# Kernel tuning notes

Hardware: AMD Instinct MI355X
Metric: run time of the kernel (lower is better)

Reference implementation:

```python
import jax, jax.numpy as jnp
import numpy as np

NUM_HEADS = 4
LN_EPS = 1e-5
NEG_INF = -1e9


def _ln(x, g, b):
    mu = jnp.mean(x, axis=-1, keepdims=True)
    var = jnp.mean(jnp.square(x - mu), axis=-1, keepdims=True)
    return (x - mu) * jax.lax.rsqrt(var + LN_EPS) * g + b


def setup_inputs() -> dict:
    key = jax.random.key(0)
    B, L, D, C, E, T, H, NL, MLP = 1024, 200, 64, 32, 32, 8, 256, 3, 256
    P = D + E            # 96
    KIN = H + 2 * T      # 272
    ks = iter(jax.random.split(key, 64))

    def w(shape, fan_in):
        return jax.random.normal(next(ks), shape, dtype=jnp.float32) / np.sqrt(fan_in)

    inp = {}
    inp['x_u'] = jax.random.normal(next(ks), (B, D), dtype=jnp.float32)
    inp['x_ctx'] = jax.random.normal(next(ks), (B, L, D), dtype=jnp.float32)
    inp['t_ctx'] = jax.random.uniform(next(ks), (B, L), dtype=jnp.float32)
    inp['act_u_idx'] = jax.random.randint(next(ks), (B,), 0, C + 1)
    inp['act_ctx_idx'] = jax.random.randint(next(ks), (B, L), 0, C + 1)
    emb = jax.random.normal(next(ks), (C + 1, E), dtype=jnp.float32)
    inp['emb'] = emb.at[0].set(0.0)  # padding_idx=0
    inp['W_in_self'] = w((P, H), P); inp['b_in_self'] = jnp.zeros((H,), jnp.float32)
    inp['W_in_ctx'] = w((P, H), P); inp['b_in_ctx'] = jnp.zeros((H,), jnp.float32)
    inp['freq'] = jax.random.normal(next(ks), (NL, T), dtype=jnp.float32)
    inp['phase'] = jnp.zeros((NL, T), jnp.float32)
    inp['Wq'] = w((NL, H, H), H)
    inp['Wk'] = w((NL, KIN, H), KIN)
    inp['Wv'] = w((NL, KIN, H), KIN)
    inp['Wres'] = w((NL, H, H), H); inp['bres'] = jnp.zeros((NL, H), jnp.float32)
    inp['Wff1'] = w((NL, H, H), H); inp['bff1'] = jnp.zeros((NL, H), jnp.float32)
    inp['Wff2'] = w((NL, H, H), H); inp['bff2'] = jnp.zeros((NL, H), jnp.float32)
    inp['g1'] = jnp.ones((NL, H), jnp.float32); inp['beta1'] = jnp.zeros((NL, H), jnp.float32)
    inp['g2'] = jnp.ones((NL, H), jnp.float32); inp['beta2'] = jnp.zeros((NL, H), jnp.float32)
    inp['W_ro'] = w((H, MLP), H); inp['b_ro'] = jnp.zeros((MLP,), jnp.float32)
    inp['W_cls'] = w((MLP, C), MLP); inp['b_cls'] = jnp.zeros((C,), jnp.float32)
    inp['W_dt'] = w((MLP, 1), MLP); inp['b_dt'] = jnp.zeros((1,), jnp.float32)
    inp['W_rem'] = w((MLP, 1), MLP); inp['b_rem'] = jnp.zeros((1,), jnp.float32)
    return inp


def reference(x_u, x_ctx, t_ctx, act_u_idx, act_ctx_idx, emb,
              W_in_self, b_in_self, W_in_ctx, b_in_ctx,
              freq, phase, Wq, Wk, Wv, Wres, bres,
              Wff1, bff1, Wff2, bff2, g1, beta1, g2, beta2,
              W_ro, b_ro, W_cls, b_cls, W_dt, b_dt, W_rem, b_rem):
    B, L, _ = x_ctx.shape
    H = W_in_self.shape[1]
    nh = NUM_HEADS
    Dh = H // nh
    scale = np.sqrt(Dh).astype(np.float32)

    mask = act_ctx_idx > 0                                   # (B, L)
    e_u = emb[act_u_idx]                                     # (B, E)
    e_ctx = emb[act_ctx_idx]                                 # (B, L, E)
    xu = jnp.concatenate([x_u, e_u], axis=-1)
    xc = jnp.concatenate([x_ctx, e_ctx], axis=-1)
    h = xu @ W_in_self + b_in_self                           # (B, H)
    ctx = xc @ W_in_ctx + b_in_ctx                           # (B, L, H)

    logt = jnp.log1p(jnp.maximum(t_ctx, 0.0))                # (B, L)
    n_layers = Wq.shape[0]
    for i in range(n_layers):
        z = logt[..., None] * freq[i] + phase[i]             # (B, L, T)
        te = jnp.concatenate([jnp.sin(z), jnp.cos(z)], axis=-1)  # (B, L, 2T)
        kv = jnp.concatenate([ctx, te], axis=-1)             # (B, L, H+2T)
        q = (h @ Wq[i]).reshape(B, nh, Dh)                   # (B, h, d)
        k = (kv @ Wk[i]).reshape(B, L, nh, Dh)               # (B, l, h, d)
        v = (kv @ Wv[i]).reshape(B, L, nh, Dh)
        att_logits = jnp.einsum('bhd,blhd->bhl', q, k) / scale
        att_logits = jnp.where(mask[:, None, :], att_logits, NEG_INF)
        att = jax.nn.softmax(att_logits, axis=-1)            # (B, h, l)
        agg = jnp.einsum('bhl,blhd->bhd', att, v).reshape(B, H)
        z1 = _ln(agg + h @ Wres[i] + bres[i], g1[i], beta1[i])
        ff = jax.nn.relu(z1 @ Wff1[i] + bff1[i]) @ Wff2[i] + bff2[i]
        h = _ln(z1 + ff, g2[i], beta2[i])

    z = jax.nn.relu(h @ W_ro + b_ro)
    logits = z @ W_cls + b_cls
    dt_hat = jax.nn.sigmoid(z @ W_dt + b_dt)
    rem_hat = jax.nn.sigmoid(z @ W_rem + b_rem)
    return (logits, dt_hat, rem_hat)
```

## Files before the change

### kernel.cpp

```cpp
#include <hip/hip_runtime.h>
#include <math.h>

namespace {
constexpr int Bc   = 1024;
constexpr int Lc   = 200;
constexpr int Dc   = 64;
constexpr int Ec   = 32;
constexpr int Pc   = 96;
constexpr int Hc   = 256;
constexpr int Tc   = 8;
constexpr int NLc  = 3;
constexpr int KINc = 272;
constexpr int DHc  = 64;
constexpr int Cc   = 32;
constexpr int QS   = 113;
constexpr int Q4   = 452;
constexpr int QP   = 464;
constexpr int CG   = 112;
constexpr int CGW  = 448;
constexpr int TEBS  = Bc * Lc + 8;
constexpr float LN_EPS_V = 1e-5f;
constexpr float NEG_BIG  = -1e9f;

typedef __attribute__((ext_vector_type(8))) short bf16x8;
typedef __attribute__((ext_vector_type(4))) float f32x4;

__device__ __forceinline__ unsigned short f2bf(float f) {
    union { float f; unsigned int u; } v; v.f = f;
    unsigned int u = v.u;
    unsigned int r = (u + 0x7fffu + ((u >> 16) & 1u)) >> 16;
    return (unsigned short)r;
}
}

__global__ __launch_bounds__(256) void k_kpv(const float* __restrict__ W_in_ctx,
                                             const float* __restrict__ b_in_ctx,
                                             const float* __restrict__ Wv,
                                             const float* __restrict__ Wk,
                                             float* __restrict__ wvp2,
                                             float* __restrict__ kp) {
    int blk = blockIdx.x;
    int i = blk / QS;
    int j = blk - i * QS;
    int t = threadIdx.x;
    __shared__ float wrow[Hc];
    if (j < 96)        wrow[t] = W_in_ctx[j * Hc + t];
    else if (j == 112) wrow[t] = b_in_ctx[t];
    __syncthreads();
    const float* WvL = Wv + (size_t)i * KINc * Hc;
    const float* WkL = Wk + (size_t)i * KINc * Hc;
    float av, ak;
    if (j >= 96 && j < 112) {
        av = WvL[(256 + (j - 96)) * Hc + t];
        ak = WkL[(256 + (j - 96)) * Hc + t];
    } else {
        av = 0.f; ak = 0.f;
        for (int c = 0; c < Hc; ++c) {
            float w = wrow[c];
            av += w * WvL[c * Hc + t];
            ak += w * WkL[c * Hc + t];
        }
    }
    wvp2[(size_t)blk * Hc + t] = av;
    kp[(size_t)blk * Hc + t]   = ak;
}

__global__ __launch_bounds__(256) void k_wbig2(const float* __restrict__ Wq,
                                               const float* __restrict__ kp,
                                               float* __restrict__ wbig) {
    __shared__ float wq_l[64][65];
    __shared__ float kp_l[113][64];
    int blk = blockIdx.x;
    int i = blk >> 4;
    int rem = blk & 15;
    int h = rem >> 2, et = rem & 3;
    int t = threadIdx.x;
    for (int idx = t; idx < 64 * 64; idx += 256) {
        int e = idx >> 6, d = idx & 63;
        wq_l[e][d] = Wq[(size_t)i * Hc * Hc + (size_t)(et * 64 + e) * Hc + h * 64 + d];
    }
    for (int idx = t; idx < 113 * 64; idx += 256) {
        int r = idx >> 6, d = idx & 63;
        kp_l[r][d] = kp[((size_t)i * QS + r) * Hc + h * 64 + d];
    }
    __syncthreads();
    int e  = t & 63;
    int rq = t >> 6;
    for (int r = rq; r < QS; r += 4) {
        float acc = 0.f;
        #pragma unroll
        for (int d = 0; d < 64; ++d) acc += wq_l[e][d] * kp_l[r][d];
        wbig[((size_t)i * Hc + et * 64 + e) * Q4 + h * QS + r] = 0.125f * acc;
    }
}

__global__ __launch_bounds__(64) void k_frag(const float* __restrict__ wvp2,
                                             const float* __restrict__ Wres,
                                             const float* __restrict__ Wff1,
                                             const float* __restrict__ Wff2,
                                             const float* __restrict__ wbig,
                                             unsigned short* __restrict__ wcat2F,
                                             unsigned short* __restrict__ wffF,
                                             unsigned short* __restrict__ wbigF) {
    int blk = blockIdx.x;
    int lane = threadIdx.x;
    unsigned short v[8];
    if (blk < NLc * 192) {
        int i = blk / 192;
        int r = blk - i * 192;
        int kk = r >> 4, ct = r & 15;
        int c = ct * 16 + (lane & 15);
        int kb = kk * 32 + (lane >> 4) * 8;
        #pragma unroll
        for (int j = 0; j < 8; ++j) {
            int k = kb + j;
            float val;
            if (k < 112)      val = wvp2[((size_t)i * QS + k) * Hc + c];
            else if (k < 368) val = Wres[(size_t)i * Hc * Hc + (size_t)(k - 112) * Hc + c];
            else              val = 0.f;
            v[j] = f2bf(val);
        }
        *(uint4*)&wcat2F[(size_t)blk * 64 * 8 + lane * 8] = *(const uint4*)v;
    } else if (blk < NLc * 192 + NLc * 256) {
        int b2 = blk - NLc * 192;
        int i = b2 / 256;
        int rem = b2 - i * 256;
        int w12 = rem >> 7;
        int r = rem & 127;
        int kk = r >> 4, ct = r & 15;
        int c = ct * 16 + (lane & 15);
        int kb = kk * 32 + (lane >> 4) * 8;
        const float* src = (w12 ? Wff2 : Wff1) + (size_t)i * Hc * Hc;
        #pragma unroll
        for (int j = 0; j < 8; ++j) v[j] = f2bf(src[(size_t)(kb + j) * Hc + c]);
        *(uint4*)&wffF[(size_t)b2 * 64 * 8 + lane * 8] = *(const uint4*)v;
    } else {
        int b3 = blk - NLc * 192 - NLc * 256;
        int i = b3 / 232;
        int r = b3 - i * 232;
        int kk = r / 29, ct = r - kk * 29;
        int c = ct * 16 + (lane & 15);
        int kb = kk * 32 + (lane >> 4) * 8;
        #pragma unroll
        for (int j = 0; j < 8; ++j) {
            float val = (c < Q4) ? wbig[((size_t)i * Hc + kb + j) * Q4 + c] : 0.f;
            v[j] = f2bf(val);
        }
        *(uint4*)&wbigF[(size_t)b3 * 64 * 8 + lane * 8] = *(const uint4*)v;
    }
}

__global__ __launch_bounds__(256) void k_h0(const float* __restrict__ x_u,
                                            const int* __restrict__ act_u,
                                            const float* __restrict__ emb,
                                            const float* __restrict__ W,
                                            const float* __restrict__ bias,
                                            float* __restrict__ h) {
    constexpr int R = 16;
    int b0 = blockIdx.x * R;
    int t = threadIdx.x;
    __shared__ float xu[R * Pc];
    for (int idx = t; idx < R * Pc; idx += 256) {
        int r = idx / Pc, j = idx - r * Pc;
        int b = b0 + r;
        float v;
        if (j < Dc) v = x_u[b * Dc + j];
        else        v = emb[act_u[b] * Ec + (j - Dc)];
        xu[idx] = v;
    }
    __syncthreads();
    float acc[R];
    float bb = bias[t];
    #pragma unroll
    for (int r = 0; r < R; ++r) acc[r] = bb;
    for (int j = 0; j < Pc; ++j) {
        float w = W[j * Hc + t];
        #pragma unroll
        for (int r = 0; r < R; ++r) acc[r] += xu[r * Pc + j] * w;
    }
    #pragma unroll
    for (int r = 0; r < R; ++r) h[(b0 + r) * Hc + t] = acc[r];
}

__global__ __launch_bounds__(256) void k_prepx(const float* __restrict__ x_ctx,
                                               const int* __restrict__ act_ctx,
                                               const float* __restrict__ emb,
                                               unsigned short* __restrict__ xtb) {
    int idx = blockIdx.x * 256 + threadIdx.x;
    int row = idx / 12, c8 = idx - row * 12;
    unsigned short v[8];
    if (c8 < 8) {
        const float* s = x_ctx + (size_t)row * Dc + c8 * 8;
        float4 a0 = *(const float4*)s;
        float4 a1 = *(const float4*)(s + 4);
        v[0]=f2bf(a0.x); v[1]=f2bf(a0.y); v[2]=f2bf(a0.z); v[3]=f2bf(a0.w);
        v[4]=f2bf(a1.x); v[5]=f2bf(a1.y); v[6]=f2bf(a1.z); v[7]=f2bf(a1.w);
    } else {
        int a = act_ctx[row];
        const float* s = emb + (size_t)a * Ec + (c8 - 8) * 8;
        float4 e0 = *(const float4*)s;
        float4 e1 = *(const float4*)(s + 4);
        v[0]=f2bf(e0.x); v[1]=f2bf(e0.y); v[2]=f2bf(e0.z); v[3]=f2bf(e0.w);
        v[4]=f2bf(e1.x); v[5]=f2bf(e1.y); v[6]=f2bf(e1.z); v[7]=f2bf(e1.w);
    }
    *(uint4*)&xtb[(size_t)row * 96 + c8 * 8] = *(const uint4*)v;
}

__global__ __launch_bounds__(256) void k_prept(const float* __restrict__ t_ctx,
                                               const float* __restrict__ freq,
                                               const float* __restrict__ phase,
                                               unsigned short* __restrict__ teb,
                                               unsigned short* __restrict__ teTb) {
    __shared__ float lt[Lc];
    int b = blockIdx.x;
    int t = threadIdx.x;
    if (t < Lc) lt[t] = log1pf(fmaxf(t_ctx[b * Lc + t], 0.f));
    __syncthreads();
    for (int idx = t; idx < NLc * Lc; idx += 256) {
        int i = idx / Lc, l = idx - i * Lc;
        float L = lt[l];
        unsigned short v[16];
        #pragma unroll
        for (int j = 0; j < 8; ++j) {
            float z = L * freq[i * Tc + j] + phase[i * Tc + j];
            v[j]     = f2bf(__sinf(z));
            v[8 + j] = f2bf(__cosf(z));
        }
        size_t base = ((size_t)i * TEBS + b * Lc + l) * 16;
        *(uint4*)&teb[base]     = *(const uint4*)v;
        *(uint4*)&teb[base + 8] = *(const uint4*)&v[8];
    }
    for (int idx = t; idx < NLc * 16 * 28; idx += 256) {
        int i  = idx / 448;
        int r2 = idx - i * 448;
        int f  = r2 / 28, ch = r2 - f * 28;
        int l0 = ch * 8;
        float fr = freq[i * Tc + (f & 7)], ph = phase[i * Tc + (f & 7)];
        bool iscos = f >= 8;
        unsigned short v[8];
        #pragma unroll
        for (int k = 0; k < 8; ++k) {
            int l = l0 + k;
            float val = 0.f;
            if (l < Lc) {
                float z = lt[l] * fr + ph;
                val = iscos ? __cosf(z) : __sinf(z);
            }
            v[k] = f2bf(val);
        }
        *(uint4*)&teTb[((size_t)i * Bc * 16 + b * 16 + f) * 224 + l0] = *(const uint4*)v;
    }
}

__global__ __launch_bounds__(256) void k_qk2b(const float* __restrict__ h,
                                              const float* __restrict__ wbig_l,
                                              unsigned short* __restrict__ qk2b) {
    constexpr int R = 4;
    int rb = blockIdx.x & 255;
    int cb = blockIdx.x >> 8;
    int b0 = rb * R;
    int t = threadIdx.x;
    int c = cb * 256 + t;
    __shared__ float hl[R * Hc];
    for (int idx = t; idx < R * Hc; idx += 256) hl[idx] = h[b0 * Hc + idx];
    __syncthreads();
    if (c >= QP) return;
    if (c >= Q4) {
        #pragma unroll
        for (int r = 0; r < R; ++r) qk2b[(size_t)(b0 + r) * QP + c] = 0;
        return;
    }
    float acc[R];
    #pragma unroll
    for (int r = 0; r < R; ++r) acc[r] = 0.f;
    for (int e = 0; e < Hc; ++e) {
        float w = wbig_l[(size_t)e * Q4 + c];
        #pragma unroll
        for (int r = 0; r < R; ++r) acc[r] += hl[r * Hc + e] * w;
    }
    #pragma unroll
    for (int r = 0; r < R; ++r) qk2b[(size_t)(b0 + r) * QP + c] = f2bf(acc[r]);
}

__global__ __launch_bounds__(512) void k_att(const int* __restrict__ act_ctx,
                                             const unsigned short* __restrict__ qk2b,
                                             const unsigned short* __restrict__ xtb,
                                             const unsigned short* __restrict__ teb_l,
                                             const unsigned short* __restrict__ teTb_l,
                                             float* __restrict__ cagg) {
    constexpr int XS = 112;
    __shared__ __align__(16) unsigned short xt[208 * XS];
    __shared__ unsigned short qks[QP];
    __shared__ float S[4][208];
    __shared__ unsigned short Pl[16][232];
    int b = blockIdx.x;
    int t = threadIdx.x;
    int wv = t >> 6, lane = t & 63;
    int kg = lane >> 4;

    if (t < QP / 2) ((unsigned int*)qks)[t] = ((const unsigned int*)(qk2b + (size_t)b * QP))[t];
    for (int idx = t; idx < 16 * 29; idx += 512) {
        int row = idx / 29, c8 = idx - row * 29;
        uint4 z = {0, 0, 0, 0};
        *(uint4*)&Pl[row][c8 * 8] = z;
    }
    const unsigned short* xrow = xtb + (size_t)b * Lc * 96;
    for (int idx = t; idx < Lc * 12; idx += 512) {
        int l = idx / 12, c8 = idx - l * 12;
        uint4 v = *(const uint4*)(xrow + (size_t)l * 96 + c8 * 8);
        *(uint4*)&xt[l * XS + c8 * 8] = v;
    }
    for (int idx = t; idx < 8 * 12; idx += 512) {
        int l = 200 + idx / 12, c8 = idx - (idx / 12) * 12;
        uint4 z = {0, 0, 0, 0};
        *(uint4*)&xt[l * XS + c8 * 8] = z;
    }
    __syncthreads();

    bf16x8 bfr[4];
    {
        int h = lane & 15;
        int kb = kg * 8;
        #pragma unroll
        for (int kk = 0; kk < 4; ++kk) {
            unsigned short tmp[8];
            #pragma unroll
            for (int j = 0; j < 8; ++j) {
                int k = kk * 32 + kb + j;
                tmp[j] = (h < 4 && k < QS) ? qks[h * QS + k] : (unsigned short)0;
            }
            bfr[kk] = *(const bf16x8*)tmp;
        }
    }

    const unsigned short* terow = teb_l + (size_t)b * Lc * 16;
    for (int tile = wv; tile < 13; tile += 8) {
        int r = tile * 16 + (lane & 15);
        bf16x8 a0 = *(const bf16x8*)&xt[r * XS + kg * 8];
        bf16x8 a1 = *(const bf16x8*)&xt[r * XS + 32 + kg * 8];
        bf16x8 a2 = *(const bf16x8*)&xt[r * XS + 64 + kg * 8];
        bf16x8 a3;
        if (kg < 2) {
            a3 = *(const bf16x8*)(terow + (size_t)r * 16 + kg * 8);
        } else if (kg == 2) {
            unsigned short tmp[8] = {0x3F80u, 0, 0, 0, 0, 0, 0, 0};
            a3 = *(const bf16x8*)tmp;
        } else {
            bf16x8 z = {0, 0, 0, 0, 0, 0, 0, 0};
            a3 = z;
        }
        f32x4 acc = {0.f, 0.f, 0.f, 0.f};
        acc = __builtin_amdgcn_mfma_f32_16x16x32_bf16(a0, bfr[0], acc, 0, 0, 0);
        acc = __builtin_amdgcn_mfma_f32_16x16x32_bf16(a1, bfr[1], acc, 0, 0, 0);
        acc = __builtin_amdgcn_mfma_f32_16x16x32_bf16(a2, bfr[2], acc, 0, 0, 0);
        acc = __builtin_amdgcn_mfma_f32_16x16x32_bf16(a3, bfr[3], acc, 0, 0, 0);
        int h = lane & 15;
        if (h < 4) {
            int rb = tile * 16 + kg * 4;
            #pragma unroll
            for (int q = 0; q < 4; ++q) S[h][rb + q] = acc[q];
        }
    }
    __syncthreads();

    if (wv < 4) {
        int h = wv;
        float lv[4];
        #pragma unroll
        for (int k = 0; k < 4; ++k) {
            int l = lane + 64 * k;
            if (l < Lc) lv[k] = (act_ctx[b * Lc + l] > 0) ? S[h][l] : NEG_BIG;
            else        lv[k] = -INFINITY;
        }
        float m = fmaxf(fmaxf(lv[0], lv[1]), fmaxf(lv[2], lv[3]));
        #pragma unroll
        for (int off = 32; off >= 1; off >>= 1) m = fmaxf(m, __shfl_xor(m, off));
        float p[4];
        float ssum = 0.f;
        #pragma unroll
        for (int k = 0; k < 4; ++k) {
            int l = lane + 64 * k;
            p[k] = (l < Lc) ? __expf(lv[k] - m) : 0.f;
            ssum += p[k];
        }
        #pragma unroll
        for (int off = 32; off >= 1; off >>= 1) ssum += __shfl_xor(ssum, off);
        float sinv = 1.f / ssum;
        #pragma unroll
        for (int k = 0; k < 4; ++k) {
            int l = lane + 64 * k;
            if (l < Lc) Pl[wv][l] = f2bf(p[k] * sinv);
        }
    }
    __syncthreads();

    const unsigned short* teT = teTb_l + (size_t)b * 16 * 224;
    if (wv < 7) {
        int tile = wv;
        int n = lane & 15;
        f32x4 acc = {0.f, 0.f, 0.f, 0.f};
        #pragma unroll
        for (int kk = 0; kk < 7; ++kk) {
            bf16x8 a = *(const bf16x8*)&Pl[lane & 15][kk * 32 + kg * 8];
            bf16x8 bb;
            if (tile < 6) {
                unsigned short tmp[8];
                #pragma unroll
                for (int jj = 0; jj < 8; ++jj)
                    tmp[jj] = xt[(kk * 32 + kg * 8 + jj) * XS + tile * 16 + n];
                bb = *(const bf16x8*)tmp;
            } else {
                bb = *(const bf16x8*)(teT + (size_t)n * 224 + kk * 32 + kg * 8);
            }
            acc = __builtin_amdgcn_mfma_f32_16x16x32_bf16(a, bb, acc, 0, 0, 0);
        }
        if (kg == 0) {
            #pragma unroll
            for (int q = 0; q < 4; ++q)
                cagg[(size_t)b * CGW + q * CG + tile * 16 + n] = acc[q];
        }
    }
}

__global__ __launch_bounds__(512) void k_postq(const float* __restrict__ cagg,
                                               float* __restrict__ h,
                                               const float* __restrict__ wvp2L,
                                               const unsigned short* __restrict__ wcat2F_l,
                                               const unsigned short* __restrict__ wff1F_l,
                                               const unsigned short* __restrict__ wff2F_l,
                                               const float* __restrict__ bresL,
                                               const float* __restrict__ bff1L,
                                               const float* __restrict__ bff2L,
                                               const float* __restrict__ g1L,
                                               const float* __restrict__ beta1L,
                                               const float* __restrict__ g2L,
                                               const float* __restrict__ beta2L,
                                               const unsigned short* __restrict__ wbigF_next,
                                               unsigned short* __restrict__ qk2b) {
    __shared__ __align__(16) unsigned short Xa[16 * 712];
    __shared__ float z1f[16 * 260];
    __shared__ __align__(16) unsigned short z1n[16 * 264];
    __shared__ __align__(16) unsigned short fb16[16 * 264];
    int r0 = blockIdx.x * 16;
    int t = threadIdx.x;
    int wv = t >> 6, lane = t & 63;
    int n = lane & 15, kg = lane >> 4;
    const bf16x8 zf = {0, 0, 0, 0, 0, 0, 0, 0};

    for (int idx = t; idx < 16 * 704; idx += 512) {
        int r = idx / 704, c = idx - r * 704;
        float v = (c < 448) ? cagg[(size_t)(r0 + r) * CGW + c]
                            : h[(size_t)(r0 + r) * Hc + (c - 448)];
        Xa[r * 712 + c] = f2bf(v);
    }
    __syncthreads();

    {
        int hh = wv >> 1;
        f32x4 acc0 = {0.f,0.f,0.f,0.f}, acc1 = {0.f,0.f,0.f,0.f};
        #pragma unroll
        for (int kk = 0; kk < 12; ++kk) {
            int k0 = kk * 32 + kg * 8;
            bf16x8 a;
            if (k0 < 112)      a = *(const bf16x8*)&Xa[(lane & 15) * 712 + hh * 112 + k0];
            else if (k0 < 368) a = *(const bf16x8*)&Xa[(lane & 15) * 712 + 448 + (k0 - 112)];
            else               a = zf;
            bf16x8 b0 = *(const bf16x8*)(wcat2F_l + (((size_t)kk * 16 + wv * 2) * 64 + lane) * 8);
            bf16x8 b1 = *(const bf16x8*)(wcat2F_l + (((size_t)kk * 16 + wv * 2 + 1) * 64 + lane) * 8);
            acc0 = __builtin_amdgcn_mfma_f32_16x16x32_bf16(a, b0, acc0, 0, 0, 0);
            acc1 = __builtin_amdgcn_mfma_f32_16x16x32_bf16(a, b1, acc1, 0, 0, 0);
        }
        int c0 = (wv * 2) * 16 + n, c1 = (wv * 2 + 1) * 16 + n;
        float bi0 = bresL[c0] + wvp2L[112 * Hc + c0];
        float bi1 = bresL[c1] + wvp2L[112 * Hc + c1];
        #pragma unroll
        for (int q = 0; q < 4; ++q) {
            z1f[(kg * 4 + q) * 260 + c0] = acc0[q] + bi0;
            z1f[(kg * 4 + q) * 260 + c1] = acc1[q] + bi1;
        }
    }
    __syncthreads();
    if (wv < 4) {
        int row = wv * 4 + kg;
        float sm = 0.f, sq = 0.f, vals[16];
        #pragma unroll
        for (int s = 0; s < 16; ++s) {
            float v = z1f[row * 260 + n + 16 * s];
            vals[s] = v; sm += v; sq += v * v;
        }
        #pragma unroll
        for (int off = 8; off >= 1; off >>= 1) { sm += __shfl_xor(sm, off); sq += __shfl_xor(sq, off); }
        float mu = sm * (1.f / 256.f);
        float rstd = rsqrtf(sq * (1.f / 256.f) - mu * mu + LN_EPS_V);
        #pragma unroll
        for (int s = 0; s < 16; ++s) {
            int c = n + 16 * s;
            float v = (vals[s] - mu) * rstd * g1L[c] + beta1L[c];
            z1f[row * 260 + c] = v;
            z1n[row * 264 + c] = f2bf(v);
        }
    }
    __syncthreads();
    {
        f32x4 acc0 = {0.f,0.f,0.f,0.f}, acc1 = {0.f,0.f,0.f,0.f};
        for (int kk = 0; kk < 8; ++kk) {
            bf16x8 a = *(const bf16x8*)&z1n[(lane & 15) * 264 + kk * 32 + kg * 8];
            bf16x8 b0 = *(const bf16x8*)(wff1F_l + (((size_t)kk * 16 + wv * 2) * 64 + lane) * 8);
            bf16x8 b1 = *(const bf16x8*)(wff1F_l + (((size_t)kk * 16 + wv * 2 + 1) * 64 + lane) * 8);
            acc0 = __builtin_amdgcn_mfma_f32_16x16x32_bf16(a, b0, acc0, 0, 0, 0);
            acc1 = __builtin_amdgcn_mfma_f32_16x16x32_bf16(a, b1, acc1, 0, 0, 0);
        }
        int c0 = (wv * 2) * 16 + n, c1 = (wv * 2 + 1) * 16 + n;
        float bi0 = bff1L[c0], bi1 = bff1L[c1];
        #pragma unroll
        for (int q = 0; q < 4; ++q) {
            fb16[(kg * 4 + q) * 264 + c0] = f2bf(fmaxf(acc0[q] + bi0, 0.f));
            fb16[(kg * 4 + q) * 264 + c1] = f2bf(fmaxf(acc1[q] + bi1, 0.f));
        }
    }
    __syncthreads();
    {
        f32x4 acc0 = {0.f,0.f,0.f,0.f}, acc1 = {0.f,0.f,0.f,0.f};
        for (int kk = 0; kk < 8; ++kk) {
            bf16x8 a = *(const bf16x8*)&fb16[(lane & 15) * 264 + kk * 32 + kg * 8];
            bf16x8 b0 = *(const bf16x8*)(wff2F_l + (((size_t)kk * 16 + wv * 2) * 64 + lane) * 8);
            bf16x8 b1 = *(const bf16x8*)(wff2F_l + (((size_t)kk * 16 + wv * 2 + 1) * 64 + lane) * 8);
            acc0 = __builtin_amdgcn_mfma_f32_16x16x32_bf16(a, b0, acc0, 0, 0, 0);
            acc1 = __builtin_amdgcn_mfma_f32_16x16x32_bf16(a, b1, acc1, 0, 0, 0);
        }
        int c0 = (wv * 2) * 16 + n, c1 = (wv * 2 + 1) * 16 + n;
        float bi0 = bff2L[c0], bi1 = bff2L[c1];
        #pragma unroll
        for (int q = 0; q < 4; ++q) {
            int row = kg * 4 + q;
            z1f[row * 260 + c0] = acc0[q] + bi0 + z1f[row * 260 + c0];
            z1f[row * 260 + c1] = acc1[q] + bi1 + z1f[row * 260 + c1];
        }
    }
    __syncthreads();
    if (wv < 4) {
        int row = wv * 4 + kg;
        float sm = 0.f, sq = 0.f, vals[16];
        #pragma unroll
        for (int s = 0; s < 16; ++s) {
            float v = z1f[row * 260 + n + 16 * s];
            vals[s] = v; sm += v; sq += v * v;
        }
        #pragma unroll
        for (int off = 8; off >= 1; off >>= 1) { sm += __shfl_xor(sm, off); sq += __shfl_xor(sq, off); }
        float mu = sm * (1.f / 256.f);
        float rstd = rsqrtf(sq * (1.f / 256.f) - mu * mu + LN_EPS_V);
        #pragma unroll
        for (int s = 0; s < 16; ++s) {
            int c = n + 16 * s;
            float v = (vals[s] - mu) * rstd * g2L[c] + beta2L[c];
            h[(size_t)(r0 + row) * Hc + c] = v;
            z1n[row * 264 + c] = f2bf(v);
        }
    }
    __syncthreads();
    if (wbigF_next) {
        for (int ct = wv; ct < 29; ct += 8) {
            f32x4 acc = {0.f, 0.f, 0.f, 0.f};
            for (int kk = 0; kk < 8; ++kk) {
                bf16x8 a = *(const bf16x8*)&z1n[(lane & 15) * 264 + kk * 32 + kg * 8];
                bf16x8 bb = *(const bf16x8*)(wbigF_next + (((size_t)kk * 29 + ct) * 64 + lane) * 8);
                acc = __builtin_amdgcn_mfma_f32_16x16x32_bf16(a, bb, acc, 0, 0, 0);
            }
            #pragma unroll
            for (int q = 0; q < 4; ++q)
                qk2b[(size_t)(r0 + kg * 4 + q) * QP + ct * 16 + n] = f2bf(acc[q]);
        }
    }
}

__global__ __launch_bounds__(256) void k_head(const float* __restrict__ h,
                                              const float* __restrict__ W_ro,
                                              const float* __restrict__ b_ro,
                                              const float* __restrict__ W_cls,
                                              const float* __restrict__ b_cls,
                                              const float* __restrict__ W_dt,
                                              const float* __restrict__ b_dt,
                                              const float* __restrict__ W_rem,
                                              const float* __restrict__ b_rem,
                                              float* __restrict__ out) {
    constexpr int R = 8;
    int b0 = blockIdx.x * R;
    int t = threadIdx.x;
    int wave = t >> 6, lane = t & 63;
    __shared__ float hl[R * Hc], zl[R * Hc];
    __shared__ float wcls[Hc * Cc];
    __shared__ float wdt[Hc], wrem[Hc];
    for (int idx = t; idx < R * Hc; idx += 256) hl[idx] = h[b0 * Hc + idx];
    for (int idx = t; idx < Hc * Cc; idx += 256) wcls[idx] = W_cls[idx];
    wdt[t] = W_dt[t];
    wrem[t] = W_rem[t];
    __syncthreads();
    float acc[R];
    float br = b_ro[t];
    #pragma unroll
    for (int r = 0; r < R; ++r) acc[r] = br;
    for (int d = 0; d < Hc; ++d) {
        float w = W_ro[d * Hc + t];
        #pragma unroll
        for (int r = 0; r < R; ++r) acc[r] += hl[r * Hc + d] * w;
    }
    #pragma unroll
    for (int r = 0; r < R; ++r) zl[r * Hc + t] = fmaxf(acc[r], 0.f);
    __syncthreads();
    {
        int rr = t >> 5;
        int c = t & 31;
        float a = b_cls[c];
        for (int d = 0; d < Hc; ++d) a += zl[rr * Hc + d] * wcls[d * Cc + c];
        out[(size_t)(b0 + rr) * Cc + c] = a;
    }
    for (int rr = wave * 2; rr < wave * 2 + 2; ++rr) {
        float sd = 0.f, sr = 0.f;
        #pragma unroll
        for (int k2 = 0; k2 < 4; ++k2) {
            float zv = zl[rr * Hc + lane + 64 * k2];
            sd += zv * wdt[lane + 64 * k2];
            sr += zv * wrem[lane + 64 * k2];
        }
        #pragma unroll
        for (int off = 32; off >= 1; off >>= 1) { sd += __shfl_xor(sd, off); sr += __shfl_xor(sr, off); }
        if (lane == 0) {
            out[(size_t)Bc * Cc + b0 + rr]      = 1.f / (1.f + __expf(-(sd + b_dt[0])));
            out[(size_t)Bc * Cc + Bc + b0 + rr] = 1.f / (1.f + __expf(-(sr + b_rem[0])));
        }
    }
}

extern "C" void kernel_launch(void* const* d_in, const int* in_sizes, int n_in,
                              void* d_out, int out_size, void* d_ws, size_t ws_size,
                              hipStream_t stream) {
    const float* x_u      = (const float*)d_in[0];
    const float* x_ctx    = (const float*)d_in[1];
    const float* t_ctx    = (const float*)d_in[2];
    const int*   act_u    = (const int*)d_in[3];
    const int*   act_ctx  = (const int*)d_in[4];
    const float* emb      = (const float*)d_in[5];
    const float* W_in_self = (const float*)d_in[6];
    const float* b_in_self = (const float*)d_in[7];
    const float* W_in_ctx  = (const float*)d_in[8];
    const float* b_in_ctx  = (const float*)d_in[9];
    const float* freq  = (const float*)d_in[10];
    const float* phase = (const float*)d_in[11];
    const float* Wq    = (const float*)d_in[12];
    const float* Wk    = (const float*)d_in[13];
    const float* Wv    = (const float*)d_in[14];
    const float* Wres  = (const float*)d_in[15];
    const float* bres  = (const float*)d_in[16];
    const float* Wff1  = (const float*)d_in[17];
    const float* bff1  = (const float*)d_in[18];
    const float* Wff2  = (const float*)d_in[19];
    const float* bff2  = (const float*)d_in[20];
    const float* g1    = (const float*)d_in[21];
    const float* beta1 = (const float*)d_in[22];
    const float* g2    = (const float*)d_in[23];
    const float* beta2 = (const float*)d_in[24];
    const float* W_ro  = (const float*)d_in[25];
    const float* b_ro  = (const float*)d_in[26];
    const float* W_cls = (const float*)d_in[27];
    const float* b_cls = (const float*)d_in[28];
    const float* W_dt  = (const float*)d_in[29];
    const float* b_dt  = (const float*)d_in[30];
    const float* W_rem = (const float*)d_in[31];
    const float* b_rem = (const float*)d_in[32];

    float* ws    = (float*)d_ws;
    float* hbuf  = ws;
    float* wbig  = hbuf  + (size_t)Bc * Hc;
    float* cagg2 = wbig  + (size_t)NLc * Hc * Q4;
    float* wvp2  = cagg2 + (size_t)Bc * CGW;
    float* kp    = wvp2  + (size_t)NLc * QS * Hc;
    unsigned short* xtb   = (unsigned short*)(kp + (size_t)NLc * QS * Hc);
    unsigned short* teb   = xtb   + (size_t)Bc * Lc * 96;
    unsigned short* teTb  = teb   + (size_t)NLc * TEBS * 16;
    unsigned short* qk2b  = teTb  + (size_t)NLc * Bc * 16 * 224;
    unsigned short* wcat2F = qk2b + (size_t)Bc * QP;
    unsigned short* wffF  = wcat2F + (size_t)NLc * 192 * 512;
    unsigned short* wbigF = wffF  + (size_t)NLc * 2 * 128 * 512;
    size_t need = ((size_t)Bc * Hc + (size_t)NLc * Hc * Q4
                  + (size_t)Bc * CGW + 2 * (size_t)NLc * QS * Hc) * 4
                + ((size_t)Bc * Lc * 96
                  + (size_t)NLc * TEBS * 16 + (size_t)NLc * Bc * 16 * 224
                  + (size_t)Bc * QP
                  + (size_t)NLc * 192 * 512 + (size_t)NLc * 2 * 128 * 512
                  + (size_t)NLc * 232 * 512) * 2;
    if (ws_size < need) return;

    float* out = (float*)d_out;

    k_kpv<<<NLc * QS, 256, 0, stream>>>(W_in_ctx, b_in_ctx, Wv, Wk, wvp2, kp);
    k_wbig2<<<NLc * 16, 256, 0, stream>>>(Wq, kp, wbig);
    k_frag<<<NLc * (192 + 256 + 232), 64, 0, stream>>>(wvp2, Wres, Wff1, Wff2, wbig,
                                                       wcat2F, wffF, wbigF);
    k_h0<<<Bc / 16, 256, 0, stream>>>(x_u, act_u, emb, W_in_self, b_in_self, hbuf);
    k_prepx<<<(Bc * Lc * 12) / 256, 256, 0, stream>>>(x_ctx, act_ctx, emb, xtb);
    k_prept<<<Bc, 256, 0, stream>>>(t_ctx, freq, phase, teb, teTb);
    k_qk2b<<<512, 256, 0, stream>>>(hbuf, wbig, qk2b);

    for (int i = 0; i < NLc; ++i) {
        k_att<<<Bc, 512, 0, stream>>>(act_ctx, qk2b, xtb,
                                      teb + (size_t)i * TEBS * 16,
                                      teTb + (size_t)i * Bc * 16 * 224, cagg2);
        const unsigned short* wbnext = (i < NLc - 1) ? (wbigF + (size_t)(i + 1) * 232 * 512)
                                                     : (const unsigned short*)nullptr;
        k_postq<<<Bc / 16, 512, 0, stream>>>(cagg2, hbuf,
                                             wvp2 + (size_t)i * QS * Hc,
                                             wcat2F + (size_t)i * 192 * 512,
                                             wffF + (size_t)(i * 2) * 128 * 512,
                                             wffF + (size_t)(i * 2 + 1) * 128 * 512,
                                             bres + i * Hc, bff1 + i * Hc, bff2 + i * Hc,
                                             g1 + i * Hc, beta1 + i * Hc,
                                             g2 + i * Hc, beta2 + i * Hc,
                                             wbnext, qk2b);
    }
    k_head<<<Bc / 8, 256, 0, stream>>>(hbuf, W_ro, b_ro, W_cls, b_cls,
                                       W_dt, b_dt, W_rem, b_rem, out);
}
```

Measured before the change: 227.6 us.

## Fuse readout head into final postq layer and merge prep kernels

Removes the separate k_head kernel by running the readout MLP, classifier and sigmoid heads inside the last k_postq layer. These use bf16 MFMA with W_ro and W_cls pre-fragmented in k_frag. It also merges k_prepx and k_prept into one per-batch k_prep kernel, cutting two launches and one round trip of h through global memory. In exchange, head matmuls now run in bf16 instead of fp32, which adds rounding error, and the prep kernel's x_ctx conversion runs with one block per batch row.

New measurement: 205.4 us. -9.7%, faster.

```diff
diff --git a/kernel.cpp b/kernel.cpp
--- a/kernel.cpp
+++ b/kernel.cpp
@@ -31,6 +31,10 @@
     unsigned int r = (u + 0x7fffu + ((u >> 16) & 1u)) >> 16;
     return (unsigned short)r;
 }
+__device__ __forceinline__ float bf2f(unsigned short us) {
+    union { unsigned int u; float f; } v; v.u = ((unsigned int)us) << 16;
+    return v.f;
+}
 }
 
 __global__ __launch_bounds__(256) void k_kpv(const float* __restrict__ W_in_ctx,
@@ -99,9 +103,13 @@
                                              const float* __restrict__ Wff1,
                                              const float* __restrict__ Wff2,
                                              const float* __restrict__ wbig,
+                                             const float* __restrict__ W_ro,
+                                             const float* __restrict__ W_cls,
                                              unsigned short* __restrict__ wcat2F,
                                              unsigned short* __restrict__ wffF,
-                                             unsigned short* __restrict__ wbigF) {
+                                             unsigned short* __restrict__ wbigF,
+                                             unsigned short* __restrict__ wroF,
+                                             unsigned short* __restrict__ wclsF) {
     int blk = blockIdx.x;
     int lane = threadIdx.x;
     unsigned short v[8];
@@ -134,7 +142,7 @@
         #pragma unroll
         for (int j = 0; j < 8; ++j) v[j] = f2bf(src[(size_t)(kb + j) * Hc + c]);
         *(uint4*)&wffF[(size_t)b2 * 64 * 8 + lane * 8] = *(const uint4*)v;
-    } else {
+    } else if (blk < NLc * 192 + NLc * 256 + NLc * 232) {
         int b3 = blk - NLc * 192 - NLc * 256;
         int i = b3 / 232;
         int r = b3 - i * 232;
@@ -147,6 +155,22 @@
             v[j] = f2bf(val);
         }
         *(uint4*)&wbigF[(size_t)b3 * 64 * 8 + lane * 8] = *(const uint4*)v;
+    } else if (blk < NLc * 192 + NLc * 256 + NLc * 232 + 128) {
+        int b4 = blk - NLc * 192 - NLc * 256 - NLc * 232;
+        int kk = b4 >> 4, ct = b4 & 15;
+        int c = ct * 16 + (lane & 15);
+        int kb = kk * 32 + (lane >> 4) * 8;
+        #pragma unroll
+        for (int j = 0; j < 8; ++j) v[j] = f2bf(W_ro[(size_t)(kb + j) * Hc + c]);
+        *(uint4*)&wroF[(size_t)b4 * 64 * 8 + lane * 8] = *(const uint4*)v;
+    } else {
+        int b5 = blk - NLc * 192 - NLc * 256 - NLc * 232 - 128;
+        int kk = b5 >> 1, ct = b5 & 1;
+        int c = ct * 16 + (lane & 15);
+        int kb = kk * 32 + (lane >> 4) * 8;
+        #pragma unroll
+        for (int j = 0; j < 8; ++j) v[j] = f2bf(W_cls[(size_t)(kb + j) * Cc + c]);
+        *(uint4*)&wclsF[(size_t)b5 * 64 * 8 + lane * 8] = *(const uint4*)v;
     }
 }
 
@@ -182,39 +206,39 @@
     for (int r = 0; r < R; ++r) h[(b0 + r) * Hc + t] = acc[r];
 }
 
-__global__ __launch_bounds__(256) void k_prepx(const float* __restrict__ x_ctx,
-                                               const int* __restrict__ act_ctx,
-                                               const float* __restrict__ emb,
-                                               unsigned short* __restrict__ xtb) {
-    int idx = blockIdx.x * 256 + threadIdx.x;
-    int row = idx / 12, c8 = idx - row * 12;
-    unsigned short v[8];
-    if (c8 < 8) {
-        const float* s = x_ctx + (size_t)row * Dc + c8 * 8;
-        float4 a0 = *(const float4*)s;
-        float4 a1 = *(const float4*)(s + 4);
-        v[0]=f2bf(a0.x); v[1]=f2bf(a0.y); v[2]=f2bf(a0.z); v[3]=f2bf(a0.w);
-        v[4]=f2bf(a1.x); v[5]=f2bf(a1.y); v[6]=f2bf(a1.z); v[7]=f2bf(a1.w);
-    } else {
-        int a = act_ctx[row];
-        const float* s = emb + (size_t)a * Ec + (c8 - 8) * 8;
-        float4 e0 = *(const float4*)s;
-        float4 e1 = *(const float4*)(s + 4);
-        v[0]=f2bf(e0.x); v[1]=f2bf(e0.y); v[2]=f2bf(e0.z); v[3]=f2bf(e0.w);
-        v[4]=f2bf(e1.x); v[5]=f2bf(e1.y); v[6]=f2bf(e1.z); v[7]=f2bf(e1.w);
-    }
-    *(uint4*)&xtb[(size_t)row * 96 + c8 * 8] = *(const uint4*)v;
-}
-
-__global__ __launch_bounds__(256) void k_prept(const float* __restrict__ t_ctx,
-                                               const float* __restrict__ freq,
-                                               const float* __restrict__ phase,
-                                               unsigned short* __restrict__ teb,
-                                               unsigned short* __restrict__ teTb) {
+__global__ __launch_bounds__(256) void k_prep(const float* __restrict__ x_ctx,
+                                              const int* __restrict__ act_ctx,
+                                              const float* __restrict__ emb,
+                                              const float* __restrict__ t_ctx,
+                                              const float* __restrict__ freq,
+                                              const float* __restrict__ phase,
+                                              unsigned short* __restrict__ xtb,
+                                              unsigned short* __restrict__ teb,
+                                              unsigned short* __restrict__ teTb) {
     __shared__ float lt[Lc];
     int b = blockIdx.x;
     int t = threadIdx.x;
     if (t < Lc) lt[t] = log1pf(fmaxf(t_ctx[b * Lc + t], 0.f));
+    for (int idx = t; idx < Lc * 12; idx += 256) {
+        int l = idx / 12, c8 = idx - l * 12;
+        int row = b * Lc + l;
+        unsigned short v[8];
+        if (c8 < 8) {
+            const float* s = x_ctx + (size_t)row * Dc + c8 * 8;
+            float4 a0 = *(const float4*)s;
+            float4 a1 = *(const float4*)(s + 4);
+            v[0]=f2bf(a0.x); v[1]=f2bf(a0.y); v[2]=f2bf(a0.z); v[3]=f2bf(a0.w);
+            v[4]=f2bf(a1.x); v[5]=f2bf(a1.y); v[6]=f2bf(a1.z); v[7]=f2bf(a1.w);
+        } else {
+            int a = act_ctx[row];
+            const float* s = emb + (size_t)a * Ec + (c8 - 8) * 8;
+            float4 e0 = *(const float4*)s;
+            float4 e1 = *(const float4*)(s + 4);
+            v[0]=f2bf(e0.x); v[1]=f2bf(e0.y); v[2]=f2bf(e0.z); v[3]=f2bf(e0.w);
+            v[4]=f2bf(e1.x); v[5]=f2bf(e1.y); v[6]=f2bf(e1.z); v[7]=f2bf(e1.w);
+        }
+        *(uint4*)&xtb[(size_t)row * 96 + c8 * 8] = *(const uint4*)v;
+    }
     __syncthreads();
     for (int idx = t; idx < NLc * Lc; idx += 256) {
         int i = idx / Lc, l = idx - i * Lc;
@@ -436,7 +460,16 @@
                                                const float* __restrict__ g2L,
                                                const float* __restrict__ beta2L,
                                                const unsigned short* __restrict__ wbigF_next,
-                                               unsigned short* __restrict__ qk2b) {
+                                               unsigned short* __restrict__ qk2b,
+                                               const unsigned short* __restrict__ wroF,
+                                               const unsigned short* __restrict__ wclsF,
+                                               const float* __restrict__ b_ro,
+                                               const float* __restrict__ b_cls,
+                                               const float* __restrict__ W_dt,
+                                               const float* __restrict__ b_dt,
+                                               const float* __restrict__ W_rem,
+                                               const float* __restrict__ b_rem,
+                                               float* __restrict__ out) {
     __shared__ __align__(16) unsigned short Xa[16 * 712];
     __shared__ float z1f[16 * 260];
     __shared__ __align__(16) unsigned short z1n[16 * 264];
@@ -571,63 +604,56 @@
             for (int q = 0; q < 4; ++q)
                 qk2b[(size_t)(r0 + kg * 4 + q) * QP + ct * 16 + n] = f2bf(acc[q]);
         }
-    }
-}
-
-__global__ __launch_bounds__(256) void k_head(const float* __restrict__ h,
-                                              const float* __restrict__ W_ro,
-                                              const float* __restrict__ b_ro,
-                                              const float* __restrict__ W_cls,
-                                              const float* __restrict__ b_cls,
-                                              const float* __restrict__ W_dt,
-                                              const float* __restrict__ b_dt,
-                                              const float* __restrict__ W_rem,
-                                              const float* __restrict__ b_rem,
-                                              float* __restrict__ out) {
-    constexpr int R = 8;
-    int b0 = blockIdx.x * R;
-    int t = threadIdx.x;
-    int wave = t >> 6, lane = t & 63;
-    __shared__ float hl[R * Hc], zl[R * Hc];
-    __shared__ float wcls[Hc * Cc];
-    __shared__ float wdt[Hc], wrem[Hc];
-    for (int idx = t; idx < R * Hc; idx += 256) hl[idx] = h[b0 * Hc + idx];
-    for (int idx = t; idx < Hc * Cc; idx += 256) wcls[idx] = W_cls[idx];
-    wdt[t] = W_dt[t];
-    wrem[t] = W_rem[t];
-    __syncthreads();
-    float acc[R];
-    float br = b_ro[t];
-    #pragma unroll
-    for (int r = 0; r < R; ++r) acc[r] = br;
-    for (int d = 0; d < Hc; ++d) {
-        float w = W_ro[d * Hc + t];
-        #pragma unroll
-        for (int r = 0; r < R; ++r) acc[r] += hl[r * Hc + d] * w;
-    }
-    #pragma unroll
-    for (int r = 0; r < R; ++r) zl[r * Hc + t] = fmaxf(acc[r], 0.f);
-    __syncthreads();
-    {
-        int rr = t >> 5;
-        int c = t & 31;
-        float a = b_cls[c];
-        for (int d = 0; d < Hc; ++d) a += zl[rr * Hc + d] * wcls[d * Cc + c];
-        out[(size_t)(b0 + rr) * Cc + c] = a;
-    }
-    for (int rr = wave * 2; rr < wave * 2 + 2; ++rr) {
-        float sd = 0.f, sr = 0.f;
-        #pragma unroll
-        for (int k2 = 0; k2 < 4; ++k2) {
-            float zv = zl[rr * Hc + lane + 64 * k2];
-            sd += zv * wdt[lane + 64 * k2];
-            sr += zv * wrem[lane + 64 * k2];
-        }
-        #pragma unroll
-        for (int off = 32; off >= 1; off >>= 1) { sd += __shfl_xor(sd, off); sr += __shfl_xor(sr, off); }
-        if (lane == 0) {
-            out[(size_t)Bc * Cc + b0 + rr]      = 1.f / (1.f + __expf(-(sd + b_dt[0])));
-            out[(size_t)Bc * Cc + Bc + b0 + rr] = 1.f / (1.f + __expf(-(sr + b_rem[0])));
+    } else {
+        {
+            f32x4 acc0 = {0.f,0.f,0.f,0.f}, acc1 = {0.f,0.f,0.f,0.f};
+            for (int kk = 0; kk < 8; ++kk) {
+                bf16x8 a = *(const bf16x8*)&z1n[(lane & 15) * 264 + kk * 32 + kg * 8];
+                bf16x8 b0 = *(const bf16x8*)(wroF + (((size_t)kk * 16 + wv * 2) * 64 + lane) * 8);
+                bf16x8 b1 = *(const bf16x8*)(wroF + (((size_t)kk * 16 + wv * 2 + 1) * 64 + lane) * 8);
+                acc0 = __builtin_amdgcn_mfma_f32_16x16x32_bf16(a, b0, acc0, 0, 0, 0);
+                acc1 = __builtin_amdgcn_mfma_f32_16x16x32_bf16(a, b1, acc1, 0, 0, 0);
+            }
+            int c0 = (wv * 2) * 16 + n, c1 = (wv * 2 + 1) * 16 + n;
+            float bi0 = b_ro[c0], bi1 = b_ro[c1];
+            #pragma unroll
+            for (int q = 0; q < 4; ++q) {
+                fb16[(kg * 4 + q) * 264 + c0] = f2bf(fmaxf(acc0[q] + bi0, 0.f));
+                fb16[(kg * 4 + q) * 264 + c1] = f2bf(fmaxf(acc1[q] + bi1, 0.f));
+            }
+        }
+        __syncthreads();
+        if (wv < 2) {
+            int ct = wv;
+            f32x4 acc = {0.f, 0.f, 0.f, 0.f};
+            for (int kk = 0; kk < 8; ++kk) {
+                bf16x8 a = *(const bf16x8*)&fb16[(lane & 15) * 264 + kk * 32 + kg * 8];
+                bf16x8 bb = *(const bf16x8*)(wclsF + (((size_t)kk * 2 + ct) * 64 + lane) * 8);
+                acc = __builtin_amdgcn_mfma_f32_16x16x32_bf16(a, bb, acc, 0, 0, 0);
+            }
+            int c = ct * 16 + n;
+            float bc = b_cls[c];
+            #pragma unroll
+            for (int q = 0; q < 4; ++q)
+                out[(size_t)(r0 + kg * 4 + q) * Cc + c] = acc[q] + bc;
+        }
+        #pragma unroll
+        for (int u = 0; u < 2; ++u) {
+            int row = wv * 2 + u;
+            float sd = 0.f, sr = 0.f;
+            #pragma unroll
+            for (int k2 = 0; k2 < 4; ++k2) {
+                int c = lane + 64 * k2;
+                float zv = bf2f(fb16[row * 264 + c]);
+                sd += zv * W_dt[c];
+                sr += zv * W_rem[c];
+            }
+            #pragma unroll
+            for (int off = 32; off >= 1; off >>= 1) { sd += __shfl_xor(sd, off); sr += __shfl_xor(sr, off); }
+            if (lane == 0) {
+                out[(size_t)Bc * Cc + (r0 + row)]      = 1.f / (1.f + __expf(-(sd + b_dt[0])));
+                out[(size_t)Bc * Cc + Bc + (r0 + row)] = 1.f / (1.f + __expf(-(sr + b_rem[0])));
+            }
         }
     }
 }
@@ -682,24 +708,26 @@
     unsigned short* wcat2F = qk2b + (size_t)Bc * QP;
     unsigned short* wffF  = wcat2F + (size_t)NLc * 192 * 512;
     unsigned short* wbigF = wffF  + (size_t)NLc * 2 * 128 * 512;
+    unsigned short* wroF  = wbigF + (size_t)NLc * 232 * 512;
+    unsigned short* wclsF = wroF  + (size_t)128 * 512;
     size_t need = ((size_t)Bc * Hc + (size_t)NLc * Hc * Q4
                   + (size_t)Bc * CGW + 2 * (size_t)NLc * QS * Hc) * 4
                 + ((size_t)Bc * Lc * 96
                   + (size_t)NLc * TEBS * 16 + (size_t)NLc * Bc * 16 * 224
                   + (size_t)Bc * QP
                   + (size_t)NLc * 192 * 512 + (size_t)NLc * 2 * 128 * 512
-                  + (size_t)NLc * 232 * 512) * 2;
+                  + (size_t)NLc * 232 * 512 + (size_t)144 * 512) * 2;
     if (ws_size < need) return;
 
     float* out = (float*)d_out;
 
     k_kpv<<<NLc * QS, 256, 0, stream>>>(W_in_ctx, b_in_ctx, Wv, Wk, wvp2, kp);
     k_wbig2<<<NLc * 16, 256, 0, stream>>>(Wq, kp, wbig);
-    k_frag<<<NLc * (192 + 256 + 232), 64, 0, stream>>>(wvp2, Wres, Wff1, Wff2, wbig,
-                                                       wcat2F, wffF, wbigF);
+    k_frag<<<NLc * (192 + 256 + 232) + 144, 64, 0, stream>>>(wvp2, Wres, Wff1, Wff2, wbig,
+                                                             W_ro, W_cls,
+                                                             wcat2F, wffF, wbigF, wroF, wclsF);
     k_h0<<<Bc / 16, 256, 0, stream>>>(x_u, act_u, emb, W_in_self, b_in_self, hbuf);
-    k_prepx<<<(Bc * Lc * 12) / 256, 256, 0, stream>>>(x_ctx, act_ctx, emb, xtb);
-    k_prept<<<Bc, 256, 0, stream>>>(t_ctx, freq, phase, teb, teTb);
+    k_prep<<<Bc, 256, 0, stream>>>(x_ctx, act_ctx, emb, t_ctx, freq, phase, xtb, teb, teTb);
     k_qk2b<<<512, 256, 0, stream>>>(hbuf, wbig, qk2b);
 
     for (int i = 0; i < NLc; ++i) {
@@ -716,8 +744,8 @@
                                              bres + i * Hc, bff1 + i * Hc, bff2 + i * Hc,
                                              g1 + i * Hc, beta1 + i * Hc,
                                              g2 + i * Hc, beta2 + i * Hc,
-                                             wbnext, qk2b);
-    }
-    k_head<<<Bc / 8, 256, 0, stream>>>(hbuf, W_ro, b_ro, W_cls, b_cls,
-                                       W_dt, b_dt, W_rem, b_rem, out);
-}
+                                             wbnext, qk2b,
+                                             wroF, wclsF, b_ro, b_cls,
+                                             W_dt, b_dt, W_rem, b_rem, out);
+    }
+}
```
